# Kernel optimization log

Measured on AMD Instinct MI355X. Metric: run time of the kernel, lower is better.

The kernel has to match this reference:

```python
import jax, jax.numpy as jnp
import numpy as np

T, HID = 2048, 1536
H, DK, DV = 12, 128, 128
KEY_DIM, VAL_DIM = H * DK, H * DV
CONV_K, GEN_RED = 4, 8
EPS = 1e-5


def setup_inputs() -> dict:
    key = jax.random.key(0)
    ks = jax.random.split(key, 12)
    def rn(k, sh, scale):
        return jax.random.normal(k, sh, dtype=jnp.float32) * scale
    inv = HID ** -0.5
    return {
        "hidden_states": rn(ks[0], (T, HID), 1.0),
        "Wq": rn(ks[1], (HID, KEY_DIM), inv),
        "Wk": rn(ks[2], (HID, KEY_DIM), inv),
        "Wv": rn(ks[3], (HID, VAL_DIM), inv),
        "Wb": rn(ks[4], (HID, H), inv),
        "Wa": rn(ks[5], (HID, H), inv),
        "A_log": jnp.log(jax.random.uniform(ks[6], (H,), minval=1e-3, maxval=16.0)),
        "dt_bias": jnp.ones((H,), jnp.float32),
        "Wg1": rn(ks[7], (HID, HID // GEN_RED), inv),
        "Wg2": rn(ks[8], (HID // GEN_RED, VAL_DIM * CONV_K), (HID // GEN_RED) ** -0.5),
        "Wgate": rn(ks[9], (HID, VAL_DIM), inv),
        "norm_weight": jnp.ones((DV,), jnp.float32),
        "Wo": rn(ks[10], (VAL_DIM, HID), VAL_DIM ** -0.5),
    }


def _dynamic_conv(v, hs, Wg1, Wg2):
    # per-token per-channel causal depthwise conv; kernels generated from hidden_states
    w = jax.nn.silu(hs @ Wg1) @ Wg2                    # (T, VAL_DIM*K)
    w = w.reshape(T, VAL_DIM, CONV_K)                  # (T, D, K)
    vpad = jnp.pad(v, ((CONV_K - 1, 0), (0, 0)))       # causal left pad
    windows = jnp.stack([vpad[i:i + T] for i in range(CONV_K)], axis=1)  # (T, K, D)
    return jax.nn.silu(jnp.einsum('tkd,tdk->td', windows, w))


def _gated_delta_rule(q, k, v, g, beta):
    # q,k: (T,H,DK); v: (T,H,DV); g,beta: (T,H)
    scale = DK ** -0.5
    def step(S, inp):
        q_t, k_t, v_t, g_t, b_t = inp
        S = S * jnp.exp(g_t)[:, None, None]            # decay state
        kv = jnp.einsum('hk,hkv->hv', k_t, S)          # k^T S
        S = S + jnp.einsum('hk,hv->hkv', k_t, (v_t - kv) * b_t[:, None])
        o_t = jnp.einsum('hk,hkv->hv', q_t, S) * scale
        return S, o_t
    S0 = jnp.zeros((H, DK, DV), jnp.float32)
    _, o = jax.lax.scan(step, S0, (q, k, v, g, beta))
    return o                                           # (T, H, DV)


def reference(hidden_states, Wq, Wk, Wv, Wb, Wa, A_log, dt_bias,
              Wg1, Wg2, Wgate, norm_weight, Wo):
    hs = hidden_states
    q = jax.nn.silu(hs @ Wq).reshape(T, H, DK)
    k = jax.nn.silu(hs @ Wk).reshape(T, H, DK)
    v = _dynamic_conv(hs @ Wv, hs, Wg1, Wg2).reshape(T, H, DV)
    beta = jax.nn.sigmoid(hs @ Wb)                           # (T, H)
    g = -jnp.exp(A_log) * jax.nn.softplus(hs @ Wa + dt_bias)  # (T, H) log-decay
    o = _gated_delta_rule(q, k, v, g, beta)                  # (T, H, DV)
    # gated RMSNorm over head_v_dim
    gate = (hs @ Wgate).reshape(T, H, DV)
    o = o * jax.lax.rsqrt(jnp.mean(o * o, axis=-1, keepdims=True) + EPS)
    o = o * norm_weight * (gate * jax.nn.sigmoid(gate))
    return o.reshape(T, VAL_DIM) @ Wo
```

## Files before the change

### kernel.cpp

```cpp
#include <hip/hip_runtime.h>
#include <hip/hip_bf16.h>
#include <math.h>

#define T     2048
#define HID   1536
#define NH    12
#define DK    128
#define DV    128
#define CONVK 4
#define CH    64
#define NC    32

typedef __attribute__((ext_vector_type(8))) short bf16x8;
typedef __attribute__((ext_vector_type(8))) _Float16 fp16x8;
typedef __attribute__((ext_vector_type(4))) float floatx4;

__device__ __forceinline__ float siluf(float x) {
    return x / (1.0f + __expf(-x));
}
__device__ __forceinline__ unsigned short f2bf(float f) {
    union { __hip_bfloat16 b; unsigned short u; } cv;
    cv.b = __float2bfloat16(f);
    return cv.u;
}
__device__ __forceinline__ float bf2f(unsigned short u) {
    union { unsigned int u; float f; } cv;
    cv.u = ((unsigned int)u) << 16;
    return cv.f;
}
__device__ __forceinline__ unsigned short f2h(float f) {
    union { _Float16 h; unsigned short u; } cv;
    cv.h = (_Float16)f;
    return cv.u;
}
__device__ __forceinline__ void gl_lds16(const void* g, void* l) {
    __builtin_amdgcn_global_load_lds(
        (const __attribute__((address_space(1))) void*)g,
        (__attribute__((address_space(3))) void*)l, 16, 0, 0);
}
__device__ __forceinline__ void split8_store(const float* xv,
                                             unsigned short* dh, unsigned short* dl) {
    ushort4 h0, h1, l0, l1;
    h0.x = f2bf(xv[0]); l0.x = f2bf(xv[0] - bf2f(h0.x));
    h0.y = f2bf(xv[1]); l0.y = f2bf(xv[1] - bf2f(h0.y));
    h0.z = f2bf(xv[2]); l0.z = f2bf(xv[2] - bf2f(h0.z));
    h0.w = f2bf(xv[3]); l0.w = f2bf(xv[3] - bf2f(h0.w));
    h1.x = f2bf(xv[4]); l1.x = f2bf(xv[4] - bf2f(h1.x));
    h1.y = f2bf(xv[5]); l1.y = f2bf(xv[5] - bf2f(h1.y));
    h1.z = f2bf(xv[6]); l1.z = f2bf(xv[6] - bf2f(h1.z));
    h1.w = f2bf(xv[7]); l1.w = f2bf(xv[7] - bf2f(h1.w));
    *(ushort4*)dh = h0; *(ushort4*)(dh + 4) = h1;
    *(ushort4*)dl = l0; *(ushort4*)(dl + 4) = l1;
}

__global__ __launch_bounds__(256) void splitcast3_kernel(const float* __restrict__ s,
                                                         unsigned short* __restrict__ hi,
                                                         unsigned short* __restrict__ lo,
                                                         unsigned short* __restrict__ h16,
                                                         int n4) {
    int i = blockIdx.x * 256 + threadIdx.x;
    if (i >= n4) return;
    float4 x = ((const float4*)s)[i];
    ushort4 h, l, f;
    h.x = f2bf(x.x); l.x = f2bf(x.x - bf2f(h.x)); f.x = f2h(x.x);
    h.y = f2bf(x.y); l.y = f2bf(x.y - bf2f(h.y)); f.y = f2h(x.y);
    h.z = f2bf(x.z); l.z = f2bf(x.z - bf2f(h.z)); f.z = f2h(x.z);
    h.w = f2bf(x.w); l.w = f2bf(x.w - bf2f(h.w)); f.w = f2h(x.w);
    ((ushort4*)hi)[i] = h;
    ((ushort4*)lo)[i] = l;
    ((ushort4*)h16)[i] = f;
}

__global__ __launch_bounds__(256) void transsplit_kernel(const float* __restrict__ src,
                                                         unsigned short* __restrict__ hi,
                                                         unsigned short* __restrict__ lo,
                                                         int K, int N) {
    __shared__ float tile[32][33];
    const int k0 = blockIdx.y * 32, n0 = blockIdx.x * 32;
    const int tx = threadIdx.x, ty = threadIdx.y;
#pragma unroll
    for (int r = 0; r < 4; ++r) {
        int kk = k0 + ty + 8 * r, nn = n0 + tx;
        tile[ty + 8 * r][tx] = (nn < N) ? src[(size_t)kk * N + nn] : 0.0f;
    }
    __syncthreads();
#pragma unroll
    for (int r = 0; r < 4; ++r) {
        int nn = n0 + ty + 8 * r, kk = k0 + tx;
        if (nn < N) {
            float x = tile[tx][ty + 8 * r];
            unsigned short h = f2bf(x);
            hi[(size_t)nn * K + kk] = h;
            lo[(size_t)nn * K + kk] = f2bf(x - bf2f(h));
        }
    }
}

__global__ __launch_bounds__(256) void transcasth_kernel(const float* __restrict__ src,
                                                         unsigned short* __restrict__ dst,
                                                         int K, int N) {
    __shared__ float tile[32][33];
    const int k0 = blockIdx.y * 32, n0 = blockIdx.x * 32;
    const int tx = threadIdx.x, ty = threadIdx.y;
#pragma unroll
    for (int r = 0; r < 4; ++r) {
        int kk = k0 + ty + 8 * r, nn = n0 + tx;
        tile[ty + 8 * r][tx] = (nn < N) ? src[(size_t)kk * N + nn] : 0.0f;
    }
    __syncthreads();
#pragma unroll
    for (int r = 0; r < 4; ++r) {
        int nn = n0 + ty + 8 * r, kk = k0 + tx;
        if (nn < N) dst[(size_t)nn * K + kk] = f2h(tile[tx][ty + 8 * r]);
    }
}

template<int EPI, int MODE>
__global__ __launch_bounds__(256)
void mgemm(const unsigned short* __restrict__ Ah, const unsigned short* __restrict__ Al,
           const unsigned short* __restrict__ Bh, const unsigned short* __restrict__ Bl,
           int K, int N, float* __restrict__ C, unsigned short* __restrict__ Cb)
{
    constexpr int BN   = MODE ? 64 : 128;
    constexpr int BCH  = BN / 16;
    constexpr int NFR  = MODE ? 2 : 4;
    __shared__ unsigned short AsH[2][4096];
    __shared__ unsigned short BsH[2][BCH * 512];
    __shared__ unsigned short AsL[MODE ? 2 : 1][MODE ? 4096 : 4];
    __shared__ unsigned short BsL[MODE ? 2 : 1][MODE ? BCH * 512 : 4];
    const int tid = threadIdx.x;
    const int wave = tid >> 6, lane = tid & 63;
    const int wr = wave >> 1, wc = wave & 1;
    const int lm = lane & 15, lq = lane >> 4;
    const int rowBase = blockIdx.y * 128, colBase = blockIdx.x * BN;

    floatx4 acc[4][NFR];
#pragma unroll
    for (int i = 0; i < 4; ++i)
#pragma unroll
        for (int j = 0; j < NFR; ++j) acc[i][j] = (floatx4){0.f, 0.f, 0.f, 0.f};

    const int mt0 = wave * 2, mt1 = wave * 2 + 1;
    const size_t aOff0 = (size_t)(rowBase + mt0 * 16 + lm) * K + lq * 8;
    const size_t aOff1 = (size_t)(rowBase + mt1 * 16 + lm) * K + lq * 8;
    const size_t bOff0 = (size_t)(colBase + mt0 * 16 + lm) * K + lq * 8;
    const size_t bOff1 = (size_t)(colBase + mt1 * 16 + lm) * K + lq * 8;
    const size_t bOffW = (size_t)(colBase + wave * 16 + lm) * K + lq * 8;

    auto STAGE = [&](int buf, int k0) {
        gl_lds16(Ah + aOff0 + k0, &AsH[buf][mt0 * 512]);
        gl_lds16(Ah + aOff1 + k0, &AsH[buf][mt1 * 512]);
        if (MODE) {
            gl_lds16(Al + aOff0 + k0, &AsL[buf][mt0 * 512]);
            gl_lds16(Al + aOff1 + k0, &AsL[buf][mt1 * 512]);
            gl_lds16(Bh + bOffW + k0, &BsH[buf][wave * 512]);
            gl_lds16(Bl + bOffW + k0, &BsL[buf][wave * 512]);
        } else {
            gl_lds16(Bh + bOff0 + k0, &BsH[buf][mt0 * 512]);
            gl_lds16(Bh + bOff1 + k0, &BsH[buf][mt1 * 512]);
        }
    };

    const int nIter = K >> 5;
    STAGE(0, 0);
    __syncthreads();
    int cur = 0;
    for (int it = 0; it < nIter; ++it) {
        if (it + 1 < nIter) STAGE(cur ^ 1, (it + 1) << 5);
        if (MODE == 0) {
            fp16x8 a[4], b[4];
#pragma unroll
            for (int i = 0; i < 4; ++i) {
                a[i] = *(const fp16x8*)&AsH[cur][(wr * 4 + i) * 512 + lane * 8];
                b[i] = *(const fp16x8*)&BsH[cur][(wc * 4 + i) * 512 + lane * 8];
            }
#pragma unroll
            for (int mi = 0; mi < 4; ++mi)
#pragma unroll
                for (int ni = 0; ni < 4; ++ni)
                    acc[mi][ni] = __builtin_amdgcn_mfma_f32_16x16x32_f16(
                        a[mi], b[ni], acc[mi][ni], 0, 0, 0);
        } else {
            bf16x8 ah[4], al[4], bh[2], bl[2];
#pragma unroll
            for (int i = 0; i < 4; ++i) {
                ah[i] = *(const bf16x8*)&AsH[cur][(wr * 4 + i) * 512 + lane * 8];
                al[i] = *(const bf16x8*)&AsL[cur][(wr * 4 + i) * 512 + lane * 8];
            }
#pragma unroll
            for (int j = 0; j < 2; ++j) {
                bh[j] = *(const bf16x8*)&BsH[cur][(wc * 2 + j) * 512 + lane * 8];
                bl[j] = *(const bf16x8*)&BsL[cur][(wc * 2 + j) * 512 + lane * 8];
            }
#pragma unroll
            for (int mi = 0; mi < 4; ++mi)
#pragma unroll
                for (int ni = 0; ni < 2; ++ni) {
                    acc[mi][ni] = __builtin_amdgcn_mfma_f32_16x16x32_bf16(
                        ah[mi], bh[ni], acc[mi][ni], 0, 0, 0);
                    acc[mi][ni] = __builtin_amdgcn_mfma_f32_16x16x32_bf16(
                        al[mi], bh[ni], acc[mi][ni], 0, 0, 0);
                    acc[mi][ni] = __builtin_amdgcn_mfma_f32_16x16x32_bf16(
                        ah[mi], bl[ni], acc[mi][ni], 0, 0, 0);
                }
        }
        __syncthreads();
        cur ^= 1;
    }

#pragma unroll
    for (int mi = 0; mi < 4; ++mi)
#pragma unroll
        for (int ni = 0; ni < NFR; ++ni) {
            const int col = colBase + wc * (NFR * 16) + ni * 16 + lm;
#pragma unroll
            for (int r = 0; r < 4; ++r) {
                const int row = rowBase + wr * 64 + mi * 16 + lq * 4 + r;
                const float x = acc[mi][ni][r];
                if (EPI == 0) C[(size_t)row * N + col] = x;
                else          Cb[(size_t)row * N + col] = f2bf(x);
            }
        }
}

__global__ __launch_bounds__(256)
void mgemm_ab(const unsigned short* __restrict__ Ah0, const unsigned short* __restrict__ Bh0,
              const unsigned short* __restrict__ Ah1, const unsigned short* __restrict__ Al1,
              const unsigned short* __restrict__ Bh1, const unsigned short* __restrict__ Bl1,
              float* __restrict__ qf, float* __restrict__ vf,
              unsigned short* __restrict__ gsilb, unsigned short* __restrict__ w1h16,
              float* __restrict__ kf, float* __restrict__ bgraw)
{
    __shared__ unsigned short smem[24576];
    const int tid = threadIdx.x;
    const int wave = tid >> 6, lane = tid & 63;
    const int wr = wave >> 1, wc = wave & 1;
    const int lm = lane & 15, lq = lane >> 4;
    const int K = 1536;
    const int bx = blockIdx.x;

    bool roleA; int aidx = 0, bidx = 0;
    if (bx < 832) { roleA = ((bx & 1) == 0); aidx = bx >> 1; bidx = bx >> 1; }
    else          { roleA = true;            aidx = 416 + (bx - 832); }

    const int mt0 = wave * 2, mt1 = wave * 2 + 1;

    if (roleA) {
        const int rowBase = (aidx / 38) * 128, colBase = (aidx % 38) * 128;
        unsigned short* AsH = smem;
        unsigned short* BsH = smem + 8192;
        floatx4 acc[4][4];
#pragma unroll
        for (int i = 0; i < 4; ++i)
#pragma unroll
            for (int j = 0; j < 4; ++j) acc[i][j] = (floatx4){0.f, 0.f, 0.f, 0.f};

        const size_t aOff0 = (size_t)(rowBase + mt0 * 16 + lm) * K + lq * 8;
        const size_t aOff1 = (size_t)(rowBase + mt1 * 16 + lm) * K + lq * 8;
        const size_t bOff0 = (size_t)(colBase + mt0 * 16 + lm) * K + lq * 8;
        const size_t bOff1 = (size_t)(colBase + mt1 * 16 + lm) * K + lq * 8;

        auto STAGE = [&](int buf, int k0) {
            gl_lds16(Ah0 + aOff0 + k0, &AsH[buf * 4096 + mt0 * 512]);
            gl_lds16(Ah0 + aOff1 + k0, &AsH[buf * 4096 + mt1 * 512]);
            gl_lds16(Bh0 + bOff0 + k0, &BsH[buf * 4096 + mt0 * 512]);
            gl_lds16(Bh0 + bOff1 + k0, &BsH[buf * 4096 + mt1 * 512]);
        };
        STAGE(0, 0);
        __syncthreads();
        int cur = 0;
        for (int it = 0; it < 48; ++it) {
            if (it + 1 < 48) STAGE(cur ^ 1, (it + 1) << 5);
            fp16x8 a[4], b[4];
#pragma unroll
            for (int i = 0; i < 4; ++i) {
                a[i] = *(const fp16x8*)&AsH[cur * 4096 + (wr * 4 + i) * 512 + lane * 8];
                b[i] = *(const fp16x8*)&BsH[cur * 4096 + (wc * 4 + i) * 512 + lane * 8];
            }
#pragma unroll
            for (int mi = 0; mi < 4; ++mi)
#pragma unroll
                for (int ni = 0; ni < 4; ++ni)
                    acc[mi][ni] = __builtin_amdgcn_mfma_f32_16x16x32_f16(
                        a[mi], b[ni], acc[mi][ni], 0, 0, 0);
            __syncthreads();
            cur ^= 1;
        }
#pragma unroll
        for (int mi = 0; mi < 4; ++mi)
#pragma unroll
            for (int ni = 0; ni < 4; ++ni) {
                const int col = colBase + wc * 64 + ni * 16 + lm;
#pragma unroll
                for (int r = 0; r < 4; ++r) {
                    const int row = rowBase + wr * 64 + mi * 16 + lq * 4 + r;
                    const float x = acc[mi][ni][r];
                    if (col < 1536)       qf[(size_t)row * 1536 + col] = siluf(x);
                    else if (col < 3072)  vf[(size_t)row * 1536 + col - 1536] = x;
                    else if (col < 4608)  gsilb[(size_t)row * 1536 + col - 3072] = f2bf(siluf(x));
                    else if (col < 4800)  w1h16[(size_t)row * 192 + col - 4608] = f2h(siluf(x));
                }
            }
    } else {
        const int rowBase = (bidx / 26) * 128, colBase = (bidx % 26) * 64;
        unsigned short* AsH = smem;
        unsigned short* AsL = smem + 8192;
        unsigned short* BsH = smem + 16384;
        unsigned short* BsL = smem + 20480;
        floatx4 acc[4][2];
#pragma unroll
        for (int i = 0; i < 4; ++i)
#pragma unroll
            for (int j = 0; j < 2; ++j) acc[i][j] = (floatx4){0.f, 0.f, 0.f, 0.f};

        const size_t aOff0 = (size_t)(rowBase + mt0 * 16 + lm) * K + lq * 8;
        const size_t aOff1 = (size_t)(rowBase + mt1 * 16 + lm) * K + lq * 8;
        const size_t bOffW = (size_t)(colBase + wave * 16 + lm) * K + lq * 8;

        auto STAGE = [&](int buf, int k0) {
            gl_lds16(Ah1 + aOff0 + k0, &AsH[buf * 4096 + mt0 * 512]);
            gl_lds16(Ah1 + aOff1 + k0, &AsH[buf * 4096 + mt1 * 512]);
            gl_lds16(Al1 + aOff0 + k0, &AsL[buf * 4096 + mt0 * 512]);
            gl_lds16(Al1 + aOff1 + k0, &AsL[buf * 4096 + mt1 * 512]);
            gl_lds16(Bh1 + bOffW + k0, &BsH[buf * 2048 + wave * 512]);
            gl_lds16(Bl1 + bOffW + k0, &BsL[buf * 2048 + wave * 512]);
        };
        STAGE(0, 0);
        __syncthreads();
        int cur = 0;
        for (int it = 0; it < 48; ++it) {
            if (it + 1 < 48) STAGE(cur ^ 1, (it + 1) << 5);
            bf16x8 ah[4], al[4], bh[2], bl[2];
#pragma unroll
            for (int i = 0; i < 4; ++i) {
                ah[i] = *(const bf16x8*)&AsH[cur * 4096 + (wr * 4 + i) * 512 + lane * 8];
                al[i] = *(const bf16x8*)&AsL[cur * 4096 + (wr * 4 + i) * 512 + lane * 8];
            }
#pragma unroll
            for (int j = 0; j < 2; ++j) {
                bh[j] = *(const bf16x8*)&BsH[cur * 2048 + (wc * 2 + j) * 512 + lane * 8];
                bl[j] = *(const bf16x8*)&BsL[cur * 2048 + (wc * 2 + j) * 512 + lane * 8];
            }
#pragma unroll
            for (int mi = 0; mi < 4; ++mi)
#pragma unroll
                for (int ni = 0; ni < 2; ++ni) {
                    acc[mi][ni] = __builtin_amdgcn_mfma_f32_16x16x32_bf16(
                        ah[mi], bh[ni], acc[mi][ni], 0, 0, 0);
                    acc[mi][ni] = __builtin_amdgcn_mfma_f32_16x16x32_bf16(
                        al[mi], bh[ni], acc[mi][ni], 0, 0, 0);
                    acc[mi][ni] = __builtin_amdgcn_mfma_f32_16x16x32_bf16(
                        ah[mi], bl[ni], acc[mi][ni], 0, 0, 0);
                }
            __syncthreads();
            cur ^= 1;
        }
#pragma unroll
        for (int mi = 0; mi < 4; ++mi)
#pragma unroll
            for (int ni = 0; ni < 2; ++ni) {
                const int col = colBase + wc * 32 + ni * 16 + lm;
#pragma unroll
                for (int r = 0; r < 4; ++r) {
                    const int row = rowBase + wr * 64 + mi * 16 + lq * 4 + r;
                    const float x = acc[mi][ni][r];
                    if (col < 1536)       kf[(size_t)row * 1536 + col] = siluf(x);
                    else if (col < 1560)  bgraw[(size_t)row * 24 + col - 1536] = x;
                }
            }
    }
}

__global__ __launch_bounds__(256) void bg2_kernel(const float* __restrict__ bgraw,
                                                  const float* __restrict__ A_log,
                                                  const float* __restrict__ dt_bias,
                                                  float* __restrict__ beta,
                                                  float* __restrict__ g) {
    int idx = blockIdx.x * 256 + threadIdx.x;
    if (idx >= T * 24) return;
    int t = idx / 24, c = idx % 24;
    float x = bgraw[idx];
    if (c < 12) {
        beta[t * NH + c] = 1.0f / (1.0f + __expf(-x));
    } else {
        int h = c - 12;
        float y = x + dt_bias[h];
        float sp = (y > 20.0f) ? y : log1pf(__expf(y));
        g[t * NH + h] = -__expf(A_log[h]) * sp;
    }
}

__global__ __launch_bounds__(256) void conv_kernel(const float* __restrict__ vpre,
                                                   const unsigned short* __restrict__ w,
                                                   float* __restrict__ v) {
    const int idx = blockIdx.x * 256 + threadIdx.x;
    if (idx >= T * HID) return;
    const int t = idx / HID, d = idx % HID;
    const ushort4 wv = *(const ushort4*)(w + (size_t)t * (HID * CONVK) + d * 4);
    const float w4[4] = { bf2f(wv.x), bf2f(wv.y), bf2f(wv.z), bf2f(wv.w) };
    float acc = 0.0f;
#pragma unroll
    for (int i = 0; i < CONVK; i++) {
        const int ts = t - (CONVK - 1) + i;
        if (ts >= 0) acc += vpre[(size_t)ts * HID + d] * w4[i];
    }
    v[idx] = siluf(acc);
}

__global__ __launch_bounds__(256) void prep_kernel(
    const float* __restrict__ q, const float* __restrict__ k,
    unsigned short* __restrict__ Qth, unsigned short* __restrict__ Qtl,
    unsigned short* __restrict__ Kth, unsigned short* __restrict__ Ktl)
{
    __shared__ float KT[128 * 68];
    const int c = blockIdx.x, h = blockIdx.y;
    const int tid = threadIdx.x;
    const size_t tb = (size_t)(h * NC + c) * 8192;

    {
        const int li = tid >> 2, lq4 = tid & 3;
        const float* src = k + (size_t)(c * CH + li) * HID + h * DK + lq4 * 32;
#pragma unroll
        for (int f = 0; f < 8; ++f) {
            float4 x = *(const float4*)(src + f * 4);
            int d0 = lq4 * 32 + f * 4;
            KT[(d0 + 0) * 68 + li] = x.x; KT[(d0 + 1) * 68 + li] = x.y;
            KT[(d0 + 2) * 68 + li] = x.z; KT[(d0 + 3) * 68 + li] = x.w;
        }
    }

#pragma unroll
    for (int e = 0; e < 4; ++e) {
        int u = e * 256 + tid;
        int ch = u >> 6, l = u & 63;
        int i = (ch >> 2) * 16 + (l & 15);
        int dbase = (ch & 3) * 32 + (l >> 4) * 8;
        const float* src = q + (size_t)(c * CH + i) * HID + h * DK + dbase;
        float4 a = *(const float4*)src, b = *(const float4*)(src + 4);
        float xv[8] = {a.x, a.y, a.z, a.w, b.x, b.y, b.z, b.w};
        split8_store(xv, &Qth[tb + ch * 512 + l * 8], &Qtl[tb + ch * 512 + l * 8]);
    }
    __syncthreads();

#pragma unroll
    for (int e = 0; e < 4; ++e) {
        int u = e * 256 + tid;
        int ch = u >> 6, l = u & 63;
        int dk = (ch >> 1) * 16 + (l & 15);
        int ibase = (ch & 1) * 32 + (l >> 4) * 8;
        float4 a = *(const float4*)&KT[dk * 68 + ibase];
        float4 b = *(const float4*)&KT[dk * 68 + ibase + 4];
        float xv[8] = {a.x, a.y, a.z, a.w, b.x, b.y, b.z, b.w};
        split8_store(xv, &Kth[tb + ch * 512 + l * 8], &Ktl[tb + ch * 512 + l * 8]);
    }
}

__global__ __launch_bounds__(256, 1) void chunkloc_kernel(
    const float* __restrict__ q, const float* __restrict__ k, const float* __restrict__ v,
    const float* __restrict__ g, const float* __restrict__ beta,
    float* __restrict__ X1g,
    unsigned short* __restrict__ X2th, unsigned short* __restrict__ X2tl,
    float* __restrict__ Mg, float* __restrict__ csg)
{
    __shared__ unsigned short KhS[64 * 136], KlS[64 * 136];
    __shared__ unsigned short QhS[64 * 136], QlS[64 * 136];
    __shared__ float KT[128 * 68];
    __shared__ float Vs[64 * 132];
    __shared__ float As[64 * 68];
    __shared__ float cs[64], sb[64], sbb[64];

    const int c = blockIdx.x, h = blockIdx.y;
    const int tid = threadIdx.x;
    const int wave = tid >> 6, lane = tid & 63;
    const int lm = lane & 15, lq = lane >> 4;
    const int li = tid >> 2, lq4 = tid & 3;
    const size_t rowbase = (size_t)(c * CH) * HID + h * DK;

    {
        const float* ksrc = k + rowbase + (size_t)li * HID + lq4 * 32;
        const float* qsrc = q + rowbase + (size_t)li * HID + lq4 * 32;
        const float* vsrc = v + (size_t)(c * CH + li) * HID + h * DV + lq4 * 32;
#pragma unroll
        for (int f = 0; f < 8; ++f) {
            float4 kx = *(const float4*)(ksrc + f * 4);
            float4 qx = *(const float4*)(qsrc + f * 4);
            float4 vx = *(const float4*)(vsrc + f * 4);
            const int d0 = lq4 * 32 + f * 4;
            {
                ushort4 hh, ll;
                hh.x = f2bf(kx.x); ll.x = f2bf(kx.x - bf2f(hh.x));
                hh.y = f2bf(kx.y); ll.y = f2bf(kx.y - bf2f(hh.y));
                hh.z = f2bf(kx.z); ll.z = f2bf(kx.z - bf2f(hh.z));
                hh.w = f2bf(kx.w); ll.w = f2bf(kx.w - bf2f(hh.w));
                *(ushort4*)&KhS[li * 136 + d0] = hh;
                *(ushort4*)&KlS[li * 136 + d0] = ll;
            }
            {
                ushort4 hh, ll;
                hh.x = f2bf(qx.x); ll.x = f2bf(qx.x - bf2f(hh.x));
                hh.y = f2bf(qx.y); ll.y = f2bf(qx.y - bf2f(hh.y));
                hh.z = f2bf(qx.z); ll.z = f2bf(qx.z - bf2f(hh.z));
                hh.w = f2bf(qx.w); ll.w = f2bf(qx.w - bf2f(hh.w));
                *(ushort4*)&QhS[li * 136 + d0] = hh;
                *(ushort4*)&QlS[li * 136 + d0] = ll;
            }
            KT[(d0 + 0) * 68 + li] = kx.x;
            KT[(d0 + 1) * 68 + li] = kx.y;
            KT[(d0 + 2) * 68 + li] = kx.z;
            KT[(d0 + 3) * 68 + li] = kx.w;
            *(float4*)&Vs[li * 132 + d0] = vx;
        }
    }
    if (tid < 64) {
        float gv = g[(c * CH + tid) * NH + h];
        float bv = beta[(c * CH + tid) * NH + h];
        float csv = gv;
#pragma unroll
        for (int off = 1; off < 64; off <<= 1) {
            float n = __shfl_up(csv, off);
            if (tid >= off) csv += n;
        }
        cs[tid] = csv; sb[tid] = bv; sbb[tid] = bv * __expf(csv);
    }
    __syncthreads();

    {
        const int ti = wave;
#pragma unroll
        for (int tj = 0; tj < 4; ++tj) {
            floatx4 acc = (floatx4){0.f, 0.f, 0.f, 0.f};
#pragma unroll
            for (int ks = 0; ks < 4; ++ks) {
                bf16x8 a_h = *(const bf16x8*)&KhS[(ti * 16 + lm) * 136 + ks * 32 + lq * 8];
                bf16x8 a_l = *(const bf16x8*)&KlS[(ti * 16 + lm) * 136 + ks * 32 + lq * 8];
                bf16x8 b_h = *(const bf16x8*)&KhS[(tj * 16 + lm) * 136 + ks * 32 + lq * 8];
                bf16x8 b_l = *(const bf16x8*)&KlS[(tj * 16 + lm) * 136 + ks * 32 + lq * 8];
                acc = __builtin_amdgcn_mfma_f32_16x16x32_bf16(a_h, b_h, acc, 0, 0, 0);
                acc = __builtin_amdgcn_mfma_f32_16x16x32_bf16(a_h, b_l, acc, 0, 0, 0);
                acc = __builtin_amdgcn_mfma_f32_16x16x32_bf16(a_l, b_h, acc, 0, 0, 0);
            }
#pragma unroll
            for (int r = 0; r < 4; ++r) {
                const int i = ti * 16 + lq * 4 + r, j = tj * 16 + lm;
                As[i * 68 + j] = (j < i) ? sb[i] * __expf(cs[i] - cs[j]) * acc[r] : 0.0f;
            }
        }
        const size_t mbase = (size_t)(h * NC + c) * CH * CH;
#pragma unroll
        for (int tj = 0; tj < 4; ++tj) {
            floatx4 acc = (floatx4){0.f, 0.f, 0.f, 0.f};
#pragma unroll
            for (int ks = 0; ks < 4; ++ks) {
                bf16x8 a_h = *(const bf16x8*)&QhS[(ti * 16 + lm) * 136 + ks * 32 + lq * 8];
                bf16x8 a_l = *(const bf16x8*)&QlS[(ti * 16 + lm) * 136 + ks * 32 + lq * 8];
                bf16x8 b_h = *(const bf16x8*)&KhS[(tj * 16 + lm) * 136 + ks * 32 + lq * 8];
                bf16x8 b_l = *(const bf16x8*)&KlS[(tj * 16 + lm) * 136 + ks * 32 + lq * 8];
                acc = __builtin_amdgcn_mfma_f32_16x16x32_bf16(a_h, b_h, acc, 0, 0, 0);
                acc = __builtin_amdgcn_mfma_f32_16x16x32_bf16(a_h, b_l, acc, 0, 0, 0);
                acc = __builtin_amdgcn_mfma_f32_16x16x32_bf16(a_l, b_h, acc, 0, 0, 0);
            }
#pragma unroll
            for (int r = 0; r < 4; ++r) {
                const int i = ti * 16 + lq * 4 + r, j = tj * 16 + lm;
                Mg[mbase + (size_t)i * 64 + j] =
                    (j <= i) ? __expf(cs[i] - cs[j]) * acc[r] : 0.0f;
            }
        }
    }

    float xc[64];
    const int col = tid;
    if (col < 128) {
#pragma unroll
        for (int i = 0; i < 64; ++i) xc[i] = sb[i] * Vs[i * 132 + col];
    } else {
        const int dcol = col - 128;
#pragma unroll
        for (int i4 = 0; i4 < 16; ++i4) {
            float4 kq = *(const float4*)&KT[dcol * 68 + i4 * 4];
            xc[i4 * 4 + 0] = sbb[i4 * 4 + 0] * kq.x;
            xc[i4 * 4 + 1] = sbb[i4 * 4 + 1] * kq.y;
            xc[i4 * 4 + 2] = sbb[i4 * 4 + 2] * kq.z;
            xc[i4 * 4 + 3] = sbb[i4 * 4 + 3] * kq.w;
        }
    }
    __syncthreads();

#pragma unroll
    for (int i = 1; i < 64; ++i) {
        float a = xc[i];
#pragma unroll
        for (int j4 = 0; j4 < (i + 3) / 4; ++j4) {
            float4 a4 = *(const float4*)&As[i * 68 + j4 * 4];
            a -= a4.x * xc[j4 * 4 + 0] + a4.y * xc[j4 * 4 + 1]
               + a4.z * xc[j4 * 4 + 2] + a4.w * xc[j4 * 4 + 3];
        }
        xc[i] = a;
    }

    {
        const size_t xbase = (size_t)(h * NC + c) * CH * 128;
        if (col < 128) {
            for (int i = 0; i < 64; ++i) X1g[xbase + (size_t)i * 128 + col] = xc[i];
        } else {
            for (int i = 0; i < 64; ++i) Vs[i * 132 + (col - 128)] = xc[i];
        }
    }
    if (tid < 64) csg[(size_t)(h * NC + c) * CH + tid] = cs[tid];
    __syncthreads();

    {
        const size_t tb = (size_t)(h * NC + c) * 8192;
#pragma unroll
        for (int e = 0; e < 4; ++e) {
            int u = e * 256 + tid;
            int ch = u >> 6, l = u & 63;
            int i = (ch >> 2) * 16 + (l & 15);
            int dbase = (ch & 3) * 32 + (l >> 4) * 8;
            float4 a = *(const float4*)&Vs[i * 132 + dbase];
            float4 b = *(const float4*)&Vs[i * 132 + dbase + 4];
            float xv[8] = {-a.x, -a.y, -a.z, -a.w, -b.x, -b.y, -b.z, -b.w};
            split8_store(xv, &X2th[tb + ch * 512 + l * 8], &X2tl[tb + ch * 512 + l * 8]);
        }
    }
}

struct StFrags {
    bf16x8 xh[4], xl[4], qh[4], ql[4], kh[4], kl[4];
    float x1r[4], csr[4], cs63;
};

__device__ __forceinline__ void st_load(
    StFrags& f,
    const unsigned short* __restrict__ Qth, const unsigned short* __restrict__ Qtl,
    const unsigned short* __restrict__ Kth, const unsigned short* __restrict__ Ktl,
    const unsigned short* __restrict__ X2th, const unsigned short* __restrict__ X2tl,
    const float* __restrict__ X1g, const float* __restrict__ csg,
    int h, int c, int db, int mw, int lane, int lq, int lm)
{
    const size_t hc = (size_t)(h * NC + c);
    const size_t xb = hc * CH * 128;
    const size_t tb = hc * 8192 + (size_t)lane * 8;
#pragma unroll
    for (int ks = 0; ks < 4; ++ks) {
        const size_t off = tb + (size_t)(mw * 4 + ks) * 512;
        f.xh[ks] = *(const bf16x8*)(X2th + off);
        f.xl[ks] = *(const bf16x8*)(X2tl + off);
        f.qh[ks] = *(const bf16x8*)(Qth + off);
        f.ql[ks] = *(const bf16x8*)(Qtl + off);
        f.kh[ks] = *(const bf16x8*)(Kth + off);
        f.kl[ks] = *(const bf16x8*)(Ktl + off);
    }
#pragma unroll
    for (int r = 0; r < 4; ++r) {
        const int row = mw * 16 + lq * 4 + r;
        f.x1r[r] = X1g[xb + (size_t)row * 128 + db * 16 + lm];
        f.csr[r] = csg[hc * CH + row];
    }
    f.cs63 = csg[hc * CH + 63];
}

__device__ __forceinline__ void st_compute(
    const StFrags& f, floatx4& st0, floatx4& st1,
    unsigned short* SBh, unsigned short* SBl,
    unsigned short* UBh, unsigned short* UBl,
    float* __restrict__ X1g, float* __restrict__ o,
    int h, int c, int db, int mw, int lane, int lq, int lm)
{
    const size_t hc = (size_t)(h * NC + c);
    const size_t xb = hc * CH * 128;

    {
        floatx4 aU0 = (floatx4){0.f, 0.f, 0.f, 0.f};
        floatx4 aU1 = (floatx4){0.f, 0.f, 0.f, 0.f};
        floatx4 aO0 = (floatx4){0.f, 0.f, 0.f, 0.f};
        floatx4 aO1 = (floatx4){0.f, 0.f, 0.f, 0.f};
#pragma unroll
        for (int ks = 0; ks < 4; ++ks) {
            bf16x8 sh = *(const bf16x8*)&SBh[lm * 136 + ks * 32 + lq * 8];
            bf16x8 sl = *(const bf16x8*)&SBl[lm * 136 + ks * 32 + lq * 8];
            if (ks & 1) {
                aU1 = __builtin_amdgcn_mfma_f32_16x16x32_bf16(f.xh[ks], sh, aU1, 0, 0, 0);
                aU1 = __builtin_amdgcn_mfma_f32_16x16x32_bf16(f.xh[ks], sl, aU1, 0, 0, 0);
                aU1 = __builtin_amdgcn_mfma_f32_16x16x32_bf16(f.xl[ks], sh, aU1, 0, 0, 0);
                aO1 = __builtin_amdgcn_mfma_f32_16x16x32_bf16(f.qh[ks], sh, aO1, 0, 0, 0);
                aO1 = __builtin_amdgcn_mfma_f32_16x16x32_bf16(f.qh[ks], sl, aO1, 0, 0, 0);
                aO1 = __builtin_amdgcn_mfma_f32_16x16x32_bf16(f.ql[ks], sh, aO1, 0, 0, 0);
            } else {
                aU0 = __builtin_amdgcn_mfma_f32_16x16x32_bf16(f.xh[ks], sh, aU0, 0, 0, 0);
                aU0 = __builtin_amdgcn_mfma_f32_16x16x32_bf16(f.xh[ks], sl, aU0, 0, 0, 0);
                aU0 = __builtin_amdgcn_mfma_f32_16x16x32_bf16(f.xl[ks], sh, aU0, 0, 0, 0);
                aO0 = __builtin_amdgcn_mfma_f32_16x16x32_bf16(f.qh[ks], sh, aO0, 0, 0, 0);
                aO0 = __builtin_amdgcn_mfma_f32_16x16x32_bf16(f.qh[ks], sl, aO0, 0, 0, 0);
                aO0 = __builtin_amdgcn_mfma_f32_16x16x32_bf16(f.ql[ks], sh, aO0, 0, 0, 0);
            }
        }
#pragma unroll
        for (int r = 0; r < 4; ++r) {
            const int row = mw * 16 + lq * 4 + r;
            const float u = aU0[r] + aU1[r] + f.x1r[r];
            X1g[xb + (size_t)row * 128 + db * 16 + lm] = u;
            const float up = u * __expf(f.cs63 - f.csr[r]);
            unsigned short uh = f2bf(up);
            UBh[lm * 72 + row] = uh;
            UBl[lm * 72 + row] = f2bf(up - bf2f(uh));
            o[(size_t)(c * CH + row) * HID + h * DV + db * 16 + lm] =
                __expf(f.csr[r]) * (aO0[r] + aO1[r]);
        }
    }
    __syncthreads();

    {
        const float bC = __expf(f.cs63);
#pragma unroll
        for (int mt2 = 0; mt2 < 2; ++mt2) {
            const int mt = mw * 2 + mt2;
            floatx4 acc;
            floatx4 stc = mt2 ? st1 : st0;
#pragma unroll
            for (int r = 0; r < 4; ++r) acc[r] = bC * stc[r];
#pragma unroll
            for (int ks = 0; ks < 2; ++ks) {
                bf16x8 ah = f.kh[mt2 * 2 + ks];
                bf16x8 al = f.kl[mt2 * 2 + ks];
                bf16x8 bh = *(const bf16x8*)&UBh[lm * 72 + ks * 32 + lq * 8];
                bf16x8 bl = *(const bf16x8*)&UBl[lm * 72 + ks * 32 + lq * 8];
                acc = __builtin_amdgcn_mfma_f32_16x16x32_bf16(ah, bh, acc, 0, 0, 0);
                acc = __builtin_amdgcn_mfma_f32_16x16x32_bf16(ah, bl, acc, 0, 0, 0);
                acc = __builtin_amdgcn_mfma_f32_16x16x32_bf16(al, bh, acc, 0, 0, 0);
            }
            if (mt2) st1 = acc; else st0 = acc;
            ushort4 shv, slv;
#pragma unroll
            for (int r = 0; r < 4; ++r) {
                const float sv = acc[r];
                unsigned short sh = f2bf(sv);
                ((unsigned short*)&shv)[r] = sh;
                ((unsigned short*)&slv)[r] = f2bf(sv - bf2f(sh));
            }
            const int dkb = mt * 16 + lq * 4;
            *(ushort4*)&SBh[lm * 136 + dkb] = shv;
            *(ushort4*)&SBl[lm * 136 + dkb] = slv;
        }
    }
    __syncthreads();
}

__global__ __launch_bounds__(256, 1) void state_kernel(
    const unsigned short* __restrict__ Qth, const unsigned short* __restrict__ Qtl,
    const unsigned short* __restrict__ Kth, const unsigned short* __restrict__ Ktl,
    const unsigned short* __restrict__ X2th, const unsigned short* __restrict__ X2tl,
    float* __restrict__ X1g ,
    const float* __restrict__ csg, float* __restrict__ o)
{
    __shared__ unsigned short SBh[16 * 136], SBl[16 * 136];
    __shared__ unsigned short UBh[16 * 72],  UBl[16 * 72];

    const int h = blockIdx.x, db = blockIdx.y;
    const int tid = threadIdx.x;
    const int mw = tid >> 6, lane = tid & 63;
    const int lm = lane & 15, lq = lane >> 4;

    for (int idx = tid; idx < 16 * 136; idx += 256) { SBh[idx] = 0; SBl[idx] = 0; }
    floatx4 st0 = (floatx4){0.f, 0.f, 0.f, 0.f};
    floatx4 st1 = (floatx4){0.f, 0.f, 0.f, 0.f};
    __syncthreads();

    StFrags fA, fB;
    st_load(fA, Qth, Qtl, Kth, Ktl, X2th, X2tl, X1g, csg, h, 0, db, mw, lane, lq, lm);
    for (int c = 0; c < NC; c += 2) {
        st_load(fB, Qth, Qtl, Kth, Ktl, X2th, X2tl, X1g, csg, h, c + 1, db, mw, lane, lq, lm);
        __builtin_amdgcn_sched_barrier(0);
        st_compute(fA, st0, st1, SBh, SBl, UBh, UBl, X1g, o, h, c, db, mw, lane, lq, lm);
        if (c + 2 < NC)
            st_load(fA, Qth, Qtl, Kth, Ktl, X2th, X2tl, X1g, csg, h, c + 2, db, mw, lane, lq, lm);
        __builtin_amdgcn_sched_barrier(0);
        st_compute(fB, st0, st1, SBh, SBl, UBh, UBl, X1g, o, h, c + 1, db, mw, lane, lq, lm);
    }
}

__global__ __launch_bounds__(256) void outk_kernel(
    const float* __restrict__ Ug, const float* __restrict__ Mg,
    float* __restrict__ o)
{
    __shared__ float Msh[64 * 68];
    __shared__ float Ush[64 * 68];

    const int c = blockIdx.x, h = blockIdx.y;
    const int dvb = blockIdx.z * 64;
    const int tid = threadIdx.x;
    const size_t hc = (size_t)(h * NC + c);

    for (int e = 0; e < 16; ++e) {
        int idx = e * 256 + tid;
        Msh[(idx >> 6) * 68 + (idx & 63)] = Mg[hc * CH * CH + idx];
    }
    for (int e = 0; e < 16; ++e) {
        int idx = e * 256 + tid;
        int j = idx >> 6, cc = idx & 63;
        Ush[j * 68 + cc] = Ug[hc * CH * 128 + (size_t)j * 128 + dvb + cc];
    }
    __syncthreads();

    const int tx = tid & 15, ty = tid >> 4;
    const int c0 = tx * 4, i0 = ty * 4;
    float acc[4][4] = {{0}};
    for (int j4 = 0; j4 < 16; ++j4) {
        float uv[4][4];
#pragma unroll
        for (int s = 0; s < 4; ++s) {
            float4 u4 = *(const float4*)&Ush[(j4 * 4 + s) * 68 + c0];
            uv[s][0] = u4.x; uv[s][1] = u4.y; uv[s][2] = u4.z; uv[s][3] = u4.w;
        }
#pragma unroll
        for (int r = 0; r < 4; ++r) {
            float4 m4 = *(const float4*)&Msh[(i0 + r) * 68 + j4 * 4];
            const float mv[4] = {m4.x, m4.y, m4.z, m4.w};
#pragma unroll
            for (int s = 0; s < 4; ++s)
#pragma unroll
                for (int e = 0; e < 4; ++e) acc[r][e] += mv[s] * uv[s][e];
        }
    }
    const float scale = 0.08838834764831845f;
#pragma unroll
    for (int r = 0; r < 4; ++r) {
        float* op = &o[(size_t)(c * CH + i0 + r) * HID + h * DV + dvb + c0];
        float4 prev = *(const float4*)op;
        float4 ov = make_float4(scale * (prev.x + acc[r][0]),
                                scale * (prev.y + acc[r][1]),
                                scale * (prev.z + acc[r][2]),
                                scale * (prev.w + acc[r][3]));
        *(float4*)op = ov;
    }
}

__global__ __launch_bounds__(256) void normgate_kernel(const float* __restrict__ o,
                                                       const unsigned short* __restrict__ gsil,
                                                       const float* __restrict__ nw,
                                                       unsigned short* __restrict__ out_hi,
                                                       unsigned short* __restrict__ out_lo) {
    const int gw = (blockIdx.x * 256 + threadIdx.x) >> 6;
    const int lane = threadIdx.x & 63;
    if (gw >= T * NH) return;
    const int t = gw / NH, h = gw % NH;
    const size_t base = (size_t)t * HID + h * DV;
    const float a = o[base + lane];
    const float b = o[base + lane + 64];
    float ss = a * a + b * b;
    ss += __shfl_xor(ss, 1);  ss += __shfl_xor(ss, 2);  ss += __shfl_xor(ss, 4);
    ss += __shfl_xor(ss, 8);  ss += __shfl_xor(ss, 16); ss += __shfl_xor(ss, 32);
    const float r = rsqrtf(ss * (1.0f / 128.0f) + 1e-5f);
    float va = a * r * nw[lane]      * bf2f(gsil[base + lane]);
    float vb = b * r * nw[lane + 64] * bf2f(gsil[base + lane + 64]);
    unsigned short ha = f2bf(va), hb = f2bf(vb);
    out_hi[base + lane]      = ha;  out_lo[base + lane]      = f2bf(va - bf2f(ha));
    out_hi[base + lane + 64] = hb;  out_lo[base + lane + 64] = f2bf(vb - bf2f(hb));
}

extern "C" void kernel_launch(void* const* d_in, const int* in_sizes, int n_in,
                              void* d_out, int out_size, void* d_ws, size_t ws_size,
                              hipStream_t stream) {
    const float* hs      = (const float*)d_in[0];
    const float* Wq      = (const float*)d_in[1];
    const float* Wk      = (const float*)d_in[2];
    const float* Wv      = (const float*)d_in[3];
    const float* Wb      = (const float*)d_in[4];
    const float* Wa      = (const float*)d_in[5];
    const float* A_log   = (const float*)d_in[6];
    const float* dt_bias = (const float*)d_in[7];
    const float* Wg1     = (const float*)d_in[8];
    const float* Wg2     = (const float*)d_in[9];
    const float* Wgate   = (const float*)d_in[10];
    const float* norm_w  = (const float*)d_in[11];
    const float* Wo      = (const float*)d_in[12];

    float* ws = (float*)d_ws;
    float* q    = ws;
    float* kbuf = ws + 3145728;
    float* vpre = ws + 6291456;
    float* vbuf = ws + 9437184;
    unsigned short* gsil = (unsigned short*)(ws + 12582912);
    float* X1g  = ws + 14155776;
    unsigned short* X2th = (unsigned short*)(ws + 17301504);
    unsigned short* X2tl = (unsigned short*)(ws + 18874368);
    float* Mg   = ws + 20447232;
    unsigned short* WTAfh = (unsigned short*)(ws + 14155776);
    unsigned short* WTBh  = (unsigned short*)(ws + 17891328);
    unsigned short* WTBl  = (unsigned short*)(ws + 19169280);
    unsigned short* wcv   = (unsigned short*)(ws + 14155776);
    unsigned short* WG2h  = (unsigned short*)(ws + 22044672);
    unsigned short* hsh   = (unsigned short*)(ws + 22634496);
    unsigned short* w1h16 = (unsigned short*)(ws + 24207360);
    float* bgraw = ws + 24403968;
    unsigned short* Kth = (unsigned short*)(ws + 22044672);
    unsigned short* Ktl = (unsigned short*)(ws + 23617536);
    float* beta  = ws + 25190400;
    float* g     = ws + 25214976;
    float* csg   = ws + 25239552;
    unsigned short* hsbh = (unsigned short*)(ws + 9437184);
    unsigned short* hsbl = (unsigned short*)(ws + 11010048);
    unsigned short* Qth  = (unsigned short*)(ws + 6291456);
    unsigned short* Qtl  = (unsigned short*)(ws + 7864320);
    unsigned short* WoTh = (unsigned short*)(ws);
    unsigned short* WoTl = (unsigned short*)(ws + 1179648);
    unsigned short* onh  = (unsigned short*)(ws + 6291456);
    unsigned short* onl  = (unsigned short*)(ws + 7864320);

    const dim3 blk(256);
    const dim3 blkT(32, 8);

    splitcast3_kernel<<<3072, blk, 0, stream>>>(hs, hsbh, hsbl, hsh, (T * HID) / 4);
    transcasth_kernel<<<dim3(48, 48), blkT, 0, stream>>>(Wq,    WTAfh,               1536, 1536);
    transcasth_kernel<<<dim3(48, 48), blkT, 0, stream>>>(Wv,    WTAfh + 1536 * 1536, 1536, 1536);
    transcasth_kernel<<<dim3(48, 48), blkT, 0, stream>>>(Wgate, WTAfh + 3072 * 1536, 1536, 1536);
    transcasth_kernel<<<dim3(6, 48),  blkT, 0, stream>>>(Wg1,   WTAfh + 4608 * 1536, 1536, 192);
    transsplit_kernel<<<dim3(48, 48), blkT, 0, stream>>>(Wk, WTBh,               WTBl,               1536, 1536);
    transsplit_kernel<<<dim3(1, 48),  blkT, 0, stream>>>(Wb, WTBh + 1536 * 1536, WTBl + 1536 * 1536, 1536, 12);
    transsplit_kernel<<<dim3(1, 48),  blkT, 0, stream>>>(Wa, WTBh + 1548 * 1536, WTBl + 1548 * 1536, 1536, 12);
    transcasth_kernel<<<dim3(192, 6), blkT, 0, stream>>>(Wg2, WG2h, 192, 6144);

    mgemm_ab<<<1024, blk, 0, stream>>>(hsh, WTAfh, hsbh, hsbl, WTBh, WTBl,
                                       q, vpre, gsil, w1h16, kbuf, bgraw);
    bg2_kernel<<<192, blk, 0, stream>>>(bgraw, A_log, dt_bias, beta, g);

    mgemm<3, 0><<<dim3(48, 16), blk, 0, stream>>>(w1h16, nullptr, WG2h, nullptr, 192, 6144,
        nullptr, wcv);
    conv_kernel<<<(T * HID) / 256, blk, 0, stream>>>(vpre, wcv, vbuf);

    chunkloc_kernel<<<dim3(NC, NH), blk, 0, stream>>>(q, kbuf, vbuf, g, beta,
                                                      X1g, X2th, X2tl, Mg, csg);
    prep_kernel<<<dim3(NC, NH), blk, 0, stream>>>(q, kbuf, Qth, Qtl, Kth, Ktl);
    state_kernel<<<dim3(NH, 8), blk, 0, stream>>>(Qth, Qtl, Kth, Ktl, X2th, X2tl,
                                                  X1g, csg, vbuf);
    transsplit_kernel<<<dim3(48, 48), blkT, 0, stream>>>(Wo, WoTh, WoTl, 1536, 1536);
    outk_kernel<<<dim3(NC, NH, 2), blk, 0, stream>>>(X1g, Mg, vbuf);

    normgate_kernel<<<6144, blk, 0, stream>>>(vbuf, gsil, norm_w, onh, onl);
    mgemm<0, 1><<<dim3(24, 16), blk, 0, stream>>>(onh, onl, WoTh, WoTl, 1536, 1536,
        (float*)d_out, nullptr);
}
```

Baseline: 539.7 us.

## Fuse beta/g activation, conv-weight GEMM with conv, and Q/K prep into neighbours

Three separate small kernels are folded into their producers. The beta/g activation moves into the mgemm_ab epilogue, so the bgraw round trip disappears. The conv-weight GEMM now applies the causal depthwise conv straight from its LDS-staged bf16 tile, so the T×HID×4 weight tensor is never written to global memory. The Q/K hi/lo transposed stores move into chunkloc, reusing data already in shared memory instead of rereading q and k. This cuts launches and global traffic, at the cost of more register and LDS pressure in the fused kernels.

```diff
diff --git a/kernel.cpp b/kernel.cpp
--- a/kernel.cpp
+++ b/kernel.cpp
@@ -229,7 +229,9 @@
               const unsigned short* __restrict__ Bh1, const unsigned short* __restrict__ Bl1,
               float* __restrict__ qf, float* __restrict__ vf,
               unsigned short* __restrict__ gsilb, unsigned short* __restrict__ w1h16,
-              float* __restrict__ kf, float* __restrict__ bgraw)
+              float* __restrict__ kf,
+              const float* __restrict__ A_log, const float* __restrict__ dt_bias,
+              float* __restrict__ beta, float* __restrict__ g)
 {
     __shared__ unsigned short smem[24576];
     const int tid = threadIdx.x;
@@ -364,94 +366,107 @@
                 for (int r = 0; r < 4; ++r) {
                     const int row = rowBase + wr * 64 + mi * 16 + lq * 4 + r;
                     const float x = acc[mi][ni][r];
-                    if (col < 1536)       kf[(size_t)row * 1536 + col] = siluf(x);
-                    else if (col < 1560)  bgraw[(size_t)row * 24 + col - 1536] = x;
+                    if (col < 1536) {
+                        kf[(size_t)row * 1536 + col] = siluf(x);
+                    } else if (col < 1560) {
+                        const int c2 = col - 1536;
+                        if (c2 < 12) {
+                            beta[row * NH + c2] = 1.0f / (1.0f + __expf(-x));
+                        } else {
+                            const int hh = c2 - 12;
+                            const float y = x + dt_bias[hh];
+                            const float sp = (y > 20.0f) ? y : log1pf(__expf(y));
+                            g[row * NH + hh] = -__expf(A_log[hh]) * sp;
+                        }
+                    }
                 }
             }
     }
 }
 
-__global__ __launch_bounds__(256) void bg2_kernel(const float* __restrict__ bgraw,
-                                                  const float* __restrict__ A_log,
-                                                  const float* __restrict__ dt_bias,
-                                                  float* __restrict__ beta,
-                                                  float* __restrict__ g) {
-    int idx = blockIdx.x * 256 + threadIdx.x;
-    if (idx >= T * 24) return;
-    int t = idx / 24, c = idx % 24;
-    float x = bgraw[idx];
-    if (c < 12) {
-        beta[t * NH + c] = 1.0f / (1.0f + __expf(-x));
-    } else {
-        int h = c - 12;
-        float y = x + dt_bias[h];
-        float sp = (y > 20.0f) ? y : log1pf(__expf(y));
-        g[t * NH + h] = -__expf(A_log[h]) * sp;
-    }
-}
-
-__global__ __launch_bounds__(256) void conv_kernel(const float* __restrict__ vpre,
-                                                   const unsigned short* __restrict__ w,
-                                                   float* __restrict__ v) {
-    const int idx = blockIdx.x * 256 + threadIdx.x;
-    if (idx >= T * HID) return;
-    const int t = idx / HID, d = idx % HID;
-    const ushort4 wv = *(const ushort4*)(w + (size_t)t * (HID * CONVK) + d * 4);
-    const float w4[4] = { bf2f(wv.x), bf2f(wv.y), bf2f(wv.z), bf2f(wv.w) };
-    float acc = 0.0f;
-#pragma unroll
-    for (int i = 0; i < CONVK; i++) {
-        const int ts = t - (CONVK - 1) + i;
-        if (ts >= 0) acc += vpre[(size_t)ts * HID + d] * w4[i];
-    }
-    v[idx] = siluf(acc);
-}
-
-__global__ __launch_bounds__(256) void prep_kernel(
-    const float* __restrict__ q, const float* __restrict__ k,
-    unsigned short* __restrict__ Qth, unsigned short* __restrict__ Qtl,
-    unsigned short* __restrict__ Kth, unsigned short* __restrict__ Ktl)
+__global__ __launch_bounds__(256)
+void convgemm(const unsigned short* __restrict__ Ah, const unsigned short* __restrict__ Bh,
+              const float* __restrict__ vpre, float* __restrict__ v)
 {
-    __shared__ float KT[128 * 68];
-    const int c = blockIdx.x, h = blockIdx.y;
+    __shared__ unsigned short smem[16384];
     const int tid = threadIdx.x;
-    const size_t tb = (size_t)(h * NC + c) * 8192;
-
-    {
-        const int li = tid >> 2, lq4 = tid & 3;
-        const float* src = k + (size_t)(c * CH + li) * HID + h * DK + lq4 * 32;
-#pragma unroll
-        for (int f = 0; f < 8; ++f) {
-            float4 x = *(const float4*)(src + f * 4);
-            int d0 = lq4 * 32 + f * 4;
-            KT[(d0 + 0) * 68 + li] = x.x; KT[(d0 + 1) * 68 + li] = x.y;
-            KT[(d0 + 2) * 68 + li] = x.z; KT[(d0 + 3) * 68 + li] = x.w;
-        }
-    }
-
-#pragma unroll
-    for (int e = 0; e < 4; ++e) {
-        int u = e * 256 + tid;
-        int ch = u >> 6, l = u & 63;
-        int i = (ch >> 2) * 16 + (l & 15);
-        int dbase = (ch & 3) * 32 + (l >> 4) * 8;
-        const float* src = q + (size_t)(c * CH + i) * HID + h * DK + dbase;
-        float4 a = *(const float4*)src, b = *(const float4*)(src + 4);
-        float xv[8] = {a.x, a.y, a.z, a.w, b.x, b.y, b.z, b.w};
-        split8_store(xv, &Qth[tb + ch * 512 + l * 8], &Qtl[tb + ch * 512 + l * 8]);
-    }
-    __syncthreads();
-
-#pragma unroll
-    for (int e = 0; e < 4; ++e) {
-        int u = e * 256 + tid;
-        int ch = u >> 6, l = u & 63;
-        int dk = (ch >> 1) * 16 + (l & 15);
-        int ibase = (ch & 1) * 32 + (l >> 4) * 8;
-        float4 a = *(const float4*)&KT[dk * 68 + ibase];
-        float4 b = *(const float4*)&KT[dk * 68 + ibase + 4];
-        float xv[8] = {a.x, a.y, a.z, a.w, b.x, b.y, b.z, b.w};
-        split8_store(xv, &Kth[tb + ch * 512 + l * 8], &Ktl[tb + ch * 512 + l * 8]);
+    const int wave = tid >> 6, lane = tid & 63;
+    const int wr = wave >> 1, wc = wave & 1;
+    const int lm = lane & 15, lq = lane >> 4;
+    const int K = 192;
+    const int rowBase = blockIdx.y * 128, colBase = blockIdx.x * 128;
+
+    unsigned short* AsH = smem;
+    unsigned short* BsH = smem + 8192;
+
+    floatx4 acc[4][4];
+#pragma unroll
+    for (int i = 0; i < 4; ++i)
+#pragma unroll
+        for (int j = 0; j < 4; ++j) acc[i][j] = (floatx4){0.f, 0.f, 0.f, 0.f};
+
+    const int mt0 = wave * 2, mt1 = wave * 2 + 1;
+    const size_t aOff0 = (size_t)(rowBase + mt0 * 16 + lm) * K + lq * 8;
+    const size_t aOff1 = (size_t)(rowBase + mt1 * 16 + lm) * K + lq * 8;
+    const size_t bOff0 = (size_t)(colBase + mt0 * 16 + lm) * K + lq * 8;
+    const size_t bOff1 = (size_t)(colBase + mt1 * 16 + lm) * K + lq * 8;
+
+    auto STAGE = [&](int buf, int k0) {
+        gl_lds16(Ah + aOff0 + k0, &AsH[buf * 4096 + mt0 * 512]);
+        gl_lds16(Ah + aOff1 + k0, &AsH[buf * 4096 + mt1 * 512]);
+        gl_lds16(Bh + bOff0 + k0, &BsH[buf * 4096 + mt0 * 512]);
+        gl_lds16(Bh + bOff1 + k0, &BsH[buf * 4096 + mt1 * 512]);
+    };
+
+    const int nIter = 6;
+    STAGE(0, 0);
+    __syncthreads();
+    int cur = 0;
+    for (int it = 0; it < nIter; ++it) {
+        if (it + 1 < nIter) STAGE(cur ^ 1, (it + 1) << 5);
+        fp16x8 a[4], b[4];
+#pragma unroll
+        for (int i = 0; i < 4; ++i) {
+            a[i] = *(const fp16x8*)&AsH[cur * 4096 + (wr * 4 + i) * 512 + lane * 8];
+            b[i] = *(const fp16x8*)&BsH[cur * 4096 + (wc * 4 + i) * 512 + lane * 8];
+        }
+#pragma unroll
+        for (int mi = 0; mi < 4; ++mi)
+#pragma unroll
+            for (int ni = 0; ni < 4; ++ni)
+                acc[mi][ni] = __builtin_amdgcn_mfma_f32_16x16x32_f16(
+                    a[mi], b[ni], acc[mi][ni], 0, 0, 0);
+        __syncthreads();
+        cur ^= 1;
+    }
+
+#pragma unroll
+    for (int mi = 0; mi < 4; ++mi)
+#pragma unroll
+        for (int ni = 0; ni < 4; ++ni) {
+            const int cl = wc * 64 + ni * 16 + lm;
+#pragma unroll
+            for (int r = 0; r < 4; ++r) {
+                const int rl = wr * 64 + mi * 16 + lq * 4 + r;
+                smem[rl * 128 + cl] = f2bf(acc[mi][ni][r]);
+            }
+        }
+    __syncthreads();
+
+    const int dB = blockIdx.x * 32;
+#pragma unroll
+    for (int e = 0; e < 16; ++e) {
+        const int u = e * 256 + tid;
+        const int tl = u >> 5, dd = u & 31;
+        const int t = rowBase + tl, d = dB + dd;
+        float a0 = 0.0f;
+#pragma unroll
+        for (int tap = 0; tap < CONVK; ++tap) {
+            const int ts = t - (CONVK - 1) + tap;
+            if (ts >= 0)
+                a0 += vpre[(size_t)ts * HID + d] * bf2f(smem[tl * 128 + dd * 4 + tap]);
+        }
+        v[(size_t)t * HID + d] = siluf(a0);
     }
 }
 
@@ -460,7 +475,9 @@
     const float* __restrict__ g, const float* __restrict__ beta,
     float* __restrict__ X1g,
     unsigned short* __restrict__ X2th, unsigned short* __restrict__ X2tl,
-    float* __restrict__ Mg, float* __restrict__ csg)
+    float* __restrict__ Mg, float* __restrict__ csg,
+    unsigned short* __restrict__ Qth, unsigned short* __restrict__ Qtl,
+    unsigned short* __restrict__ Kth, unsigned short* __restrict__ Ktl)
 {
     __shared__ unsigned short KhS[64 * 136], KlS[64 * 136];
     __shared__ unsigned short QhS[64 * 136], QlS[64 * 136];
@@ -609,8 +626,9 @@
     if (tid < 64) csg[(size_t)(h * NC + c) * CH + tid] = cs[tid];
     __syncthreads();
 
+    const size_t tb = (size_t)(h * NC + c) * 8192;
+
     {
-        const size_t tb = (size_t)(h * NC + c) * 8192;
 #pragma unroll
         for (int e = 0; e < 4; ++e) {
             int u = e * 256 + tid;
@@ -621,6 +639,32 @@
             float4 b = *(const float4*)&Vs[i * 132 + dbase + 4];
             float xv[8] = {-a.x, -a.y, -a.z, -a.w, -b.x, -b.y, -b.z, -b.w};
             split8_store(xv, &X2th[tb + ch * 512 + l * 8], &X2tl[tb + ch * 512 + l * 8]);
+        }
+    }
+
+    {
+#pragma unroll
+        for (int e = 0; e < 4; ++e) {
+            int u = e * 256 + tid;
+            int ch = u >> 6, l = u & 63;
+            int i = (ch >> 2) * 16 + (l & 15);
+            int dbase = (ch & 3) * 32 + (l >> 4) * 8;
+            *(bf16x8*)&Qth[tb + ch * 512 + l * 8] = *(const bf16x8*)&QhS[i * 136 + dbase];
+            *(bf16x8*)&Qtl[tb + ch * 512 + l * 8] = *(const bf16x8*)&QlS[i * 136 + dbase];
+        }
+    }
+
+    {
+#pragma unroll
+        for (int e = 0; e < 4; ++e) {
+            int u = e * 256 + tid;
+            int ch = u >> 6, l = u & 63;
+            int dk = (ch >> 1) * 16 + (l & 15);
+            int ibase = (ch & 1) * 32 + (l >> 4) * 8;
+            float4 a = *(const float4*)&KT[dk * 68 + ibase];
+            float4 b = *(const float4*)&KT[dk * 68 + ibase + 4];
+            float xv[8] = {a.x, a.y, a.z, a.w, b.x, b.y, b.z, b.w};
+            split8_store(xv, &Kth[tb + ch * 512 + l * 8], &Ktl[tb + ch * 512 + l * 8]);
         }
     }
 }
@@ -888,11 +932,9 @@
     unsigned short* WTAfh = (unsigned short*)(ws + 14155776);
     unsigned short* WTBh  = (unsigned short*)(ws + 17891328);
     unsigned short* WTBl  = (unsigned short*)(ws + 19169280);
-    unsigned short* wcv   = (unsigned short*)(ws + 14155776);
     unsigned short* WG2h  = (unsigned short*)(ws + 22044672);
     unsigned short* hsh   = (unsigned short*)(ws + 22634496);
     unsigned short* w1h16 = (unsigned short*)(ws + 24207360);
-    float* bgraw = ws + 24403968;
     unsigned short* Kth = (unsigned short*)(ws + 22044672);
     unsigned short* Ktl = (unsigned short*)(ws + 23617536);
     float* beta  = ws + 25190400;
@@ -921,16 +963,14 @@
     transcasth_kernel<<<dim3(192, 6), blkT, 0, stream>>>(Wg2, WG2h, 192, 6144);
 
     mgemm_ab<<<1024, blk, 0, stream>>>(hsh, WTAfh, hsbh, hsbl, WTBh, WTBl,
-                                       q, vpre, gsil, w1h16, kbuf, bgraw);
-    bg2_kernel<<<192, blk, 0, stream>>>(bgraw, A_log, dt_bias, beta, g);
-
-    mgemm<3, 0><<<dim3(48, 16), blk, 0, stream>>>(w1h16, nullptr, WG2h, nullptr, 192, 6144,
-        nullptr, wcv);
-    conv_kernel<<<(T * HID) / 256, blk, 0, stream>>>(vpre, wcv, vbuf);
+                                       q, vpre, gsil, w1h16, kbuf,
+                                       A_log, dt_bias, beta, g);
+
+    convgemm<<<dim3(48, 16), blk, 0, stream>>>(w1h16, WG2h, vpre, vbuf);
 
     chunkloc_kernel<<<dim3(NC, NH), blk, 0, stream>>>(q, kbuf, vbuf, g, beta,
-                                                      X1g, X2th, X2tl, Mg, csg);
-    prep_kernel<<<dim3(NC, NH), blk, 0, stream>>>(q, kbuf, Qth, Qtl, Kth, Ktl);
+                                                      X1g, X2th, X2tl, Mg, csg,
+                                                      Qth, Qtl, Kth, Ktl);
     state_kernel<<<dim3(NH, 8), blk, 0, stream>>>(Qth, Qtl, Kth, Ktl, X2th, X2tl,
                                                   X1g, csg, vbuf);
     transsplit_kernel<<<dim3(48, 48), blkT, 0, stream>>>(Wo, WoTh, WoTl, 1536, 1536);
```

Result: slower. 551.6 us (+2.2%).
